# Kernel tuning notes

Measured on AMD Instinct MI355X. Metric: run time of the kernel, lower is better.

The kernel has to match this reference:

```python
import jax, jax.numpy as jnp
import numpy as np
from jax import lax

ALPHA = 0.85
C1 = 0.01 ** 2
C2 = 0.03 ** 2


def _avg_pool3(x):
    # F.avg_pool2d(x, 3, 1, 1) with count_include_pad=True: zero-pad, divide by 9.
    s = lax.reduce_window(x, jnp.array(0.0, x.dtype), lax.add,
                          (1, 1, 3, 3), (1, 1, 1, 1),
                          [(0, 0), (0, 0), (1, 1), (1, 1)])
    return s / jnp.array(9.0, x.dtype)


def _ssim(x, y):
    mu_x = _avg_pool3(x)
    mu_y = _avg_pool3(y)
    sigma_x = jnp.clip(_avg_pool3(x * x) - mu_x * mu_x, 0.0, None)
    sigma_y = jnp.clip(_avg_pool3(y * y) - mu_y * mu_y, 0.0, None)
    sigma_xy = _avg_pool3(x * y) - mu_x * mu_y
    ssim_n = (2.0 * mu_x * mu_y + C1) * (2.0 * sigma_xy + C2)
    ssim_d = (mu_x * mu_x + mu_y * mu_y + C1) * (sigma_x + sigma_y + C2)
    return jnp.clip((1.0 - ssim_n / ssim_d) / 2.0, 0.0, 1.0)


def _warp_right(right_img, disp):
    # grid_sample(bilinear, border, align_corners=True) where y maps identically
    # to its own row -> a 1D horizontal bilinear gather at x_sample = x - disp.
    B, C, H, W = right_img.shape
    x_base = jnp.arange(W, dtype=disp.dtype).reshape(1, 1, 1, W)
    x_sample = x_base - disp                      # [B,1,H,W]
    xs = jnp.clip(x_sample, 0.0, W - 1.0)         # border padding
    x0 = jnp.floor(xs)
    w = xs - x0                                   # frac weight
    i0 = x0.astype(jnp.int32)
    i1 = jnp.minimum(i0 + 1, W - 1)
    i0b = jnp.broadcast_to(i0, (B, C, H, W))
    i1b = jnp.broadcast_to(i1, (B, C, H, W))
    g0 = jnp.take_along_axis(right_img, i0b, axis=3)
    g1 = jnp.take_along_axis(right_img, i1b, axis=3)
    warped = (1.0 - w) * g0 + w * g1              # w broadcasts over C
    valid = ((x_sample > 0) & (x_sample < W - 1)).astype(disp.dtype)
    return warped, valid


def setup_inputs() -> dict:
    key = jax.random.key(0)
    k1, k2, k3 = jax.random.split(key, 3)
    B, H, W = 8, 720, 1280
    disp = jax.random.normal(k1, (B, 1, H, W), dtype=jnp.float32)
    left_img = jax.random.uniform(k2, (B, 3, H, W), dtype=jnp.float32)
    right_img = jax.random.uniform(k3, (B, 3, H, W), dtype=jnp.float32)
    return {"disp": disp, "left_img": left_img, "right_img": right_img}


def reference(disp, left_img, right_img):
    right_warped, valid = _warp_right(right_img, disp)
    l1_err = jnp.mean(jnp.abs(left_img - right_warped), axis=1, keepdims=True)
    ssim_err = jnp.mean(_ssim(left_img, right_warped), axis=1, keepdims=True)
    photo_err = ALPHA * ssim_err + (1.0 - ALPHA) * l1_err
    n_valid = jnp.maximum(jnp.sum(valid), 1.0)
    return jnp.sum(photo_err * valid) / n_valid
```

## Files before the change

### kernel.cpp

```cpp
#include <hip/hip_runtime.h>


#define P_ALPHA 0.85f
#define P_C1 1e-4f
#define P_C2 9e-4f

constexpr int COLS  = 62;
constexpr int RPW   = 15;
constexpr int WAVES = 4;

__global__ __launch_bounds__(256, 4)
void photo_loss_kernel(const float* __restrict__ disp,
                       const float* __restrict__ left,
                       const float* __restrict__ right,
                       float* __restrict__ acc,
                       int H, int W)
{
    __shared__ float redpv[WAVES];
    __shared__ float redv[WAVES];

    const int tid  = threadIdx.x;
    const int lane = tid & 63;
    const int w    = tid >> 6;
    const int b    = blockIdx.z;
    const int col  = blockIdx.x * COLS + lane - 1;
    const int rowStart = (blockIdx.y * WAVES + w) * RPW;

    const int planeHW = H * W;
    const float* __restrict__ dispb = disp  + b * planeHW;
    const float* __restrict__ L0 = left  + (b * 3 + 0) * planeHW;
    const float* __restrict__ L1 = left  + (b * 3 + 1) * planeHW;
    const float* __restrict__ L2 = left  + (b * 3 + 2) * planeHW;
    const float* __restrict__ R0 = right + (b * 3 + 0) * planeHW;
    const float* __restrict__ R1 = right + (b * 3 + 1) * planeHW;
    const float* __restrict__ R2 = right + (b * 3 + 2) * planeHW;

    const float wm1f = (float)(W - 1);
    const int   colC = min(max(col, 0), W - 1);
    const float colv = (col >= 0 && col < W) ? 1.f : 0.f;
    const float ocm  = (lane >= 1 && lane <= COLS && col < W) ? 1.f : 0.f;

    float rsx[3][3], rsy[3][3], rsxx[3][3], rsyy[3][3], rsxy[3][3];
    float l1r[3], vr[3];

    float sum_pv = 0.f, sum_v = 0.f;

    auto emit = [&](int cs) {
        const float inv9 = 1.f / 9.f;
        float ssim_sum = 0.f;
        #pragma unroll
        for (int c = 0; c < 3; ++c) {
            float mu_x = (rsx[c][0]  + rsx[c][1]  + rsx[c][2])  * inv9;
            float mu_y = (rsy[c][0]  + rsy[c][1]  + rsy[c][2])  * inv9;
            float exx  = (rsxx[c][0] + rsxx[c][1] + rsxx[c][2]) * inv9;
            float eyy  = (rsyy[c][0] + rsyy[c][1] + rsyy[c][2]) * inv9;
            float exy  = (rsxy[c][0] + rsxy[c][1] + rsxy[c][2]) * inv9;
            float sig_x  = fmaxf(exx - mu_x * mu_x, 0.f);
            float sig_y  = fmaxf(eyy - mu_y * mu_y, 0.f);
            float sig_xy = exy - mu_x * mu_y;
            float n  = (2.f * mu_x * mu_y + P_C1) * (2.f * sig_xy + P_C2);
            float dd = (mu_x * mu_x + mu_y * mu_y + P_C1) * (sig_x + sig_y + P_C2);
            float s  = (1.f - n * __builtin_amdgcn_rcpf(dd)) * 0.5f;
            s = fminf(fmaxf(s, 0.f), 1.f);
            ssim_sum += s;
        }
        float photo = P_ALPHA * (ssim_sum * (1.f / 3.f))
                    + (1.f - P_ALPHA) * (l1r[cs] * (1.f / 3.f));
        sum_pv += photo * vr[cs] * ocm;
        sum_v  += vr[cs] * ocm;
    };

    float gC0,gC1,gC2,gC3,gC4,gC5, frC, vmC;
    float xC0,xC1,xC2;
    float dN;
    int   offN;

    {
        const int r0   = rowStart - 1;
        const int rc0  = max(r0, 0);
        const int off0 = rc0 * W + colC;
        const float d0 = dispb[off0];
        xC0 = L0[off0]; xC1 = L1[off0]; xC2 = L2[off0];
        offN = rowStart * W + colC;
        dN = dispb[offN];
        const float xs  = (float)col - d0;
        const float xcl = fminf(fmaxf(xs, 0.f), wm1f);
        const float xf  = floorf(xcl);
        frC = xcl - xf;
        const int i0 = (int)xf;
        const int i1 = min(i0 + 1, W - 1);
        const int ro = rc0 * W;
        gC0 = R0[ro + i0]; gC1 = R0[ro + i1];
        gC2 = R1[ro + i0]; gC3 = R1[ro + i1];
        gC4 = R2[ro + i0]; gC5 = R2[ro + i1];
        vmC = (xs > 0.f && xs < wm1f) ? 1.f : 0.f;
    }

    #pragma unroll
    for (int j = 0; j <= RPW + 2; ++j) {
        const int s = j % 3;
        const int r = rowStart - 1 + j;
        if (j <= RPW + 1) {
            float gN0=0.f,gN1=0.f,gN2=0.f,gN3=0.f,gN4=0.f,gN5=0.f, frN=0.f, vmN=0.f;
            float xN0=0.f,xN1=0.f,xN2=0.f, dF=0.f;
            int   offF = 0;
            if (j <= RPW) {
                const float xs  = (float)col - dN;
                const float xcl = fminf(fmaxf(xs, 0.f), wm1f);
                const float xf  = floorf(xcl);
                frN = xcl - xf;
                const int i0 = (int)xf;
                const int i1 = min(i0 + 1, W - 1);
                const int ro = offN - colC;
                gN0 = R0[ro + i0]; gN1 = R0[ro + i1];
                gN2 = R1[ro + i0]; gN3 = R1[ro + i1];
                gN4 = R2[ro + i0]; gN5 = R2[ro + i1];
                vmN = (xs > 0.f && xs < wm1f) ? 1.f : 0.f;

                xN0 = L0[offN]; xN1 = L1[offN]; xN2 = L2[offN];
                const int rc2 = min(r + 2, H - 1);
                offF = rc2 * W + colC;
                dF = dispb[offF];
            }

            if (j >= 3) emit((s + 1) % 3);

            const float rv = (r >= 0 && r < H) ? 1.f : 0.f;
            const float m  = rv * colv;
            const float omf = 1.f - frC;
            const float y0 = (omf * gC0 + frC * gC1) * m;
            const float y1 = (omf * gC2 + frC * gC3) * m;
            const float y2 = (omf * gC4 + frC * gC5) * m;
            const float x0 = xC0 * m;
            const float x1 = xC1 * m;
            const float x2 = xC2 * m;

            float xl, xr, yl, yr;
            xl = __shfl_up(x0, 1, 64); xr = __shfl_down(x0, 1, 64);
            yl = __shfl_up(y0, 1, 64); yr = __shfl_down(y0, 1, 64);
            rsx[0][s]  = xl + x0 + xr;
            rsy[0][s]  = yl + y0 + yr;
            rsxx[0][s] = xl * xl + x0 * x0 + xr * xr;
            rsyy[0][s] = yl * yl + y0 * y0 + yr * yr;
            rsxy[0][s] = xl * yl + x0 * y0 + xr * yr;

            xl = __shfl_up(x1, 1, 64); xr = __shfl_down(x1, 1, 64);
            yl = __shfl_up(y1, 1, 64); yr = __shfl_down(y1, 1, 64);
            rsx[1][s]  = xl + x1 + xr;
            rsy[1][s]  = yl + y1 + yr;
            rsxx[1][s] = xl * xl + x1 * x1 + xr * xr;
            rsyy[1][s] = yl * yl + y1 * y1 + yr * yr;
            rsxy[1][s] = xl * yl + x1 * y1 + xr * yr;

            xl = __shfl_up(x2, 1, 64); xr = __shfl_down(x2, 1, 64);
            yl = __shfl_up(y2, 1, 64); yr = __shfl_down(y2, 1, 64);
            rsx[2][s]  = xl + x2 + xr;
            rsy[2][s]  = yl + y2 + yr;
            rsxx[2][s] = xl * xl + x2 * x2 + xr * xr;
            rsyy[2][s] = yl * yl + y2 * y2 + yr * yr;
            rsxy[2][s] = xl * yl + x2 * y2 + xr * yr;

            l1r[s] = fabsf(x0 - y0) + fabsf(x1 - y1) + fabsf(x2 - y2);
            vr[s]  = vmC;

            if (j <= RPW) {
                gC0 = gN0; gC1 = gN1; gC2 = gN2; gC3 = gN3; gC4 = gN4; gC5 = gN5;
                frC = frN; vmC = vmN;
                xC0 = xN0; xC1 = xN1; xC2 = xN2;
                dN = dF; offN = offF;
            }
        } else {
            emit((s + 1) % 3);
        }
    }

    #pragma unroll
    for (int off = 32; off > 0; off >>= 1) {
        sum_pv += __shfl_down(sum_pv, off, 64);
        sum_v  += __shfl_down(sum_v,  off, 64);
    }
    if (lane == 0) { redpv[w] = sum_pv; redv[w] = sum_v; }
    __syncthreads();
    if (tid == 0) {
        atomicAdd(&acc[0], redpv[0] + redpv[1] + redpv[2] + redpv[3]);
        atomicAdd(&acc[1], redv[0]  + redv[1]  + redv[2]  + redv[3]);
    }
}

__global__ void photo_loss_finalize(const float* __restrict__ acc,
                                    float* __restrict__ out)
{
    out[0] = acc[0] / fmaxf(acc[1], 1.f);
}

extern "C" void kernel_launch(void* const* d_in, const int* in_sizes, int n_in,
                              void* d_out, int out_size, void* d_ws, size_t ws_size,
                              hipStream_t stream)
{
    const float* disp  = (const float*)d_in[0];
    const float* left  = (const float*)d_in[1];
    const float* right = (const float*)d_in[2];
    float* out = (float*)d_out;
    float* acc = (float*)d_ws;

    const int B = 8, H = 720, W = 1280;

    hipMemsetAsync(acc, 0, 2 * sizeof(float), stream);

    dim3 grid((W + COLS - 1) / COLS, H / (WAVES * RPW), B);
    dim3 block(256);
    photo_loss_kernel<<<grid, block, 0, stream>>>(disp, left, right, acc, H, W);
    photo_loss_finalize<<<1, 1, 0, stream>>>(acc, out);
}
```

Measured before the change: 239.7 us.

## Restructure row loop as rolling named-register window with partial unroll and higher occupancy

Replaces the fully unrolled 3-slot ring buffer of row sums with explicit A/B/C named register sets that shift each iteration, uses unroll 2 instead of full unroll, and emits SSIM for the middle row as soon as the current row is computed. The launch bound is raised to 6 blocks per SIMD-group target to force lower register use and more waves in flight for latency hiding of the gather loads. Risks include extra register moves per iteration, possible spilling under the tighter bound, and loop overhead from partial unrolling.

```diff
diff --git a/kernel.cpp b/kernel.cpp
--- a/kernel.cpp
+++ b/kernel.cpp
@@ -9,7 +9,7 @@
 constexpr int RPW   = 15;
 constexpr int WAVES = 4;
 
-__global__ __launch_bounds__(256, 4)
+__global__ __launch_bounds__(256, 6)
 void photo_loss_kernel(const float* __restrict__ disp,
                        const float* __restrict__ left,
                        const float* __restrict__ right,
@@ -40,138 +40,145 @@
     const float colv = (col >= 0 && col < W) ? 1.f : 0.f;
     const float ocm  = (lane >= 1 && lane <= COLS && col < W) ? 1.f : 0.f;
 
-    float rsx[3][3], rsy[3][3], rsxx[3][3], rsyy[3][3], rsxy[3][3];
-    float l1r[3], vr[3];
+    float Ax0=0.f,Ay0=0.f,Axx0=0.f,Ayy0=0.f,Axy0=0.f;
+    float Ax1=0.f,Ay1=0.f,Axx1=0.f,Ayy1=0.f,Axy1=0.f;
+    float Ax2=0.f,Ay2=0.f,Axx2=0.f,Ayy2=0.f,Axy2=0.f;
+    float Bx0=0.f,By0=0.f,Bxx0=0.f,Byy0=0.f,Bxy0=0.f;
+    float Bx1=0.f,By1=0.f,Bxx1=0.f,Byy1=0.f,Bxy1=0.f;
+    float Bx2=0.f,By2=0.f,Bxx2=0.f,Byy2=0.f,Bxy2=0.f;
+    float l1P=0.f, vP=0.f;
 
     float sum_pv = 0.f, sum_v = 0.f;
 
-    auto emit = [&](int cs) {
-        const float inv9 = 1.f / 9.f;
-        float ssim_sum = 0.f;
-        #pragma unroll
-        for (int c = 0; c < 3; ++c) {
-            float mu_x = (rsx[c][0]  + rsx[c][1]  + rsx[c][2])  * inv9;
-            float mu_y = (rsy[c][0]  + rsy[c][1]  + rsy[c][2])  * inv9;
-            float exx  = (rsxx[c][0] + rsxx[c][1] + rsxx[c][2]) * inv9;
-            float eyy  = (rsyy[c][0] + rsyy[c][1] + rsyy[c][2]) * inv9;
-            float exy  = (rsxy[c][0] + rsxy[c][1] + rsxy[c][2]) * inv9;
-            float sig_x  = fmaxf(exx - mu_x * mu_x, 0.f);
-            float sig_y  = fmaxf(eyy - mu_y * mu_y, 0.f);
-            float sig_xy = exy - mu_x * mu_y;
-            float n  = (2.f * mu_x * mu_y + P_C1) * (2.f * sig_xy + P_C2);
-            float dd = (mu_x * mu_x + mu_y * mu_y + P_C1) * (sig_x + sig_y + P_C2);
-            float s  = (1.f - n * __builtin_amdgcn_rcpf(dd)) * 0.5f;
-            s = fminf(fmaxf(s, 0.f), 1.f);
-            ssim_sum += s;
-        }
-        float photo = P_ALPHA * (ssim_sum * (1.f / 3.f))
-                    + (1.f - P_ALPHA) * (l1r[cs] * (1.f / 3.f));
-        sum_pv += photo * vr[cs] * ocm;
-        sum_v  += vr[cs] * ocm;
-    };
-
-    float gC0,gC1,gC2,gC3,gC4,gC5, frC, vmC;
-    float xC0,xC1,xC2;
+    float gN0,gN1,gN2,gN3,gN4,gN5, frN, vmN, xN0,xN1,xN2;
     float dN;
     int   offN;
 
     {
-        const int r0   = rowStart - 1;
-        const int rc0  = max(r0, 0);
-        const int off0 = rc0 * W + colC;
-        const float d0 = dispb[off0];
-        xC0 = L0[off0]; xC1 = L1[off0]; xC2 = L2[off0];
+        const int   rc0  = max(rowStart - 1, 0);
+        const int   off0 = rc0 * W + colC;
+        const float d0   = dispb[off0];
+        xN0 = L0[off0]; xN1 = L1[off0]; xN2 = L2[off0];
         offN = rowStart * W + colC;
-        dN = dispb[offN];
+        dN   = dispb[offN];
         const float xs  = (float)col - d0;
         const float xcl = fminf(fmaxf(xs, 0.f), wm1f);
         const float xf  = floorf(xcl);
-        frC = xcl - xf;
+        frN = xcl - xf;
         const int i0 = (int)xf;
         const int i1 = min(i0 + 1, W - 1);
         const int ro = rc0 * W;
-        gC0 = R0[ro + i0]; gC1 = R0[ro + i1];
-        gC2 = R1[ro + i0]; gC3 = R1[ro + i1];
-        gC4 = R2[ro + i0]; gC5 = R2[ro + i1];
-        vmC = (xs > 0.f && xs < wm1f) ? 1.f : 0.f;
-    }
-
-    #pragma unroll
-    for (int j = 0; j <= RPW + 2; ++j) {
-        const int s = j % 3;
+        gN0 = R0[ro + i0]; gN1 = R0[ro + i1];
+        gN2 = R1[ro + i0]; gN3 = R1[ro + i1];
+        gN4 = R2[ro + i0]; gN5 = R2[ro + i1];
+        vmN = (xs > 0.f && xs < wm1f) ? 1.f : 0.f;
+    }
+
+    #pragma unroll 2
+    for (int j = 0; j < RPW + 2; ++j) {
         const int r = rowStart - 1 + j;
-        if (j <= RPW + 1) {
-            float gN0=0.f,gN1=0.f,gN2=0.f,gN3=0.f,gN4=0.f,gN5=0.f, frN=0.f, vmN=0.f;
-            float xN0=0.f,xN1=0.f,xN2=0.f, dF=0.f;
-            int   offF = 0;
-            if (j <= RPW) {
-                const float xs  = (float)col - dN;
-                const float xcl = fminf(fmaxf(xs, 0.f), wm1f);
-                const float xf  = floorf(xcl);
-                frN = xcl - xf;
-                const int i0 = (int)xf;
-                const int i1 = min(i0 + 1, W - 1);
-                const int ro = offN - colC;
-                gN0 = R0[ro + i0]; gN1 = R0[ro + i1];
-                gN2 = R1[ro + i0]; gN3 = R1[ro + i1];
-                gN4 = R2[ro + i0]; gN5 = R2[ro + i1];
-                vmN = (xs > 0.f && xs < wm1f) ? 1.f : 0.f;
-
-                xN0 = L0[offN]; xN1 = L1[offN]; xN2 = L2[offN];
-                const int rc2 = min(r + 2, H - 1);
-                offF = rc2 * W + colC;
-                dF = dispb[offF];
+
+        const float g0=gN0,g1=gN1,g2=gN2,g3=gN3,g4=gN4,g5=gN5;
+        const float fr=frN, vm=vmN, xc0=xN0, xc1=xN1, xc2=xN2;
+
+        if (j <= RPW) {
+            const float xs  = (float)col - dN;
+            const float xcl = fminf(fmaxf(xs, 0.f), wm1f);
+            const float xf  = floorf(xcl);
+            frN = xcl - xf;
+            const int i0 = (int)xf;
+            const int i1 = min(i0 + 1, W - 1);
+            const int ro = offN - colC;
+            gN0 = R0[ro + i0]; gN1 = R0[ro + i1];
+            gN2 = R1[ro + i0]; gN3 = R1[ro + i1];
+            gN4 = R2[ro + i0]; gN5 = R2[ro + i1];
+            vmN = (xs > 0.f && xs < wm1f) ? 1.f : 0.f;
+            xN0 = L0[offN]; xN1 = L1[offN]; xN2 = L2[offN];
+            const int rc2 = min(r + 2, H - 1);
+            offN = rc2 * W + colC;
+            dN   = dispb[offN];
+        }
+
+        const float rv  = (r >= 0 && r < H) ? 1.f : 0.f;
+        const float m   = rv * colv;
+        const float omf = 1.f - fr;
+        const float y0 = (omf * g0 + fr * g1) * m;
+        const float y1 = (omf * g2 + fr * g3) * m;
+        const float y2 = (omf * g4 + fr * g5) * m;
+        const float x0 = xc0 * m;
+        const float x1 = xc1 * m;
+        const float x2 = xc2 * m;
+
+        float Cx0,Cy0,Cxx0,Cyy0,Cxy0;
+        float Cx1,Cy1,Cxx1,Cyy1,Cxy1;
+        float Cx2,Cy2,Cxx2,Cyy2,Cxy2;
+        {
+            const float xl = __shfl_up(x0,1,64), xr = __shfl_down(x0,1,64);
+            const float yl = __shfl_up(y0,1,64), yr = __shfl_down(y0,1,64);
+            Cx0  = xl + x0 + xr;
+            Cy0  = yl + y0 + yr;
+            Cxx0 = xl*xl + x0*x0 + xr*xr;
+            Cyy0 = yl*yl + y0*y0 + yr*yr;
+            Cxy0 = xl*yl + x0*y0 + xr*yr;
+        }
+        {
+            const float xl = __shfl_up(x1,1,64), xr = __shfl_down(x1,1,64);
+            const float yl = __shfl_up(y1,1,64), yr = __shfl_down(y1,1,64);
+            Cx1  = xl + x1 + xr;
+            Cy1  = yl + y1 + yr;
+            Cxx1 = xl*xl + x1*x1 + xr*xr;
+            Cyy1 = yl*yl + y1*y1 + yr*yr;
+            Cxy1 = xl*yl + x1*y1 + xr*yr;
+        }
+        {
+            const float xl = __shfl_up(x2,1,64), xr = __shfl_down(x2,1,64);
+            const float yl = __shfl_up(y2,1,64), yr = __shfl_down(y2,1,64);
+            Cx2  = xl + x2 + xr;
+            Cy2  = yl + y2 + yr;
+            Cxx2 = xl*xl + x2*x2 + xr*xr;
+            Cyy2 = yl*yl + y2*y2 + yr*yr;
+            Cxy2 = xl*yl + x2*y2 + xr*yr;
+        }
+        const float l1C = fabsf(x0 - y0) + fabsf(x1 - y1) + fabsf(x2 - y2);
+        const float vC  = vm;
+
+        if (j >= 2) {
+            const float inv9 = 1.f / 9.f;
+            float ssim_sum = 0.f;
+            #define SSIM_CH(SX,SY,SXX,SYY,SXY)                                   \
+            {                                                                    \
+                const float mu_x = (A##SX + B##SX + C##SX) * inv9;               \
+                const float mu_y = (A##SY + B##SY + C##SY) * inv9;               \
+                const float exx  = (A##SXX + B##SXX + C##SXX) * inv9;            \
+                const float eyy  = (A##SYY + B##SYY + C##SYY) * inv9;            \
+                const float exy  = (A##SXY + B##SXY + C##SXY) * inv9;            \
+                const float sig_x  = fmaxf(exx - mu_x * mu_x, 0.f);              \
+                const float sig_y  = fmaxf(eyy - mu_y * mu_y, 0.f);              \
+                const float sig_xy = exy - mu_x * mu_y;                          \
+                const float n  = (2.f*mu_x*mu_y + P_C1) * (2.f*sig_xy + P_C2);   \
+                const float dd = (mu_x*mu_x + mu_y*mu_y + P_C1)                  \
+                               * (sig_x + sig_y + P_C2);                         \
+                float s = (1.f - n * __builtin_amdgcn_rcpf(dd)) * 0.5f;          \
+                s = fminf(fmaxf(s, 0.f), 1.f);                                   \
+                ssim_sum += s;                                                   \
             }
-
-            if (j >= 3) emit((s + 1) % 3);
-
-            const float rv = (r >= 0 && r < H) ? 1.f : 0.f;
-            const float m  = rv * colv;
-            const float omf = 1.f - frC;
-            const float y0 = (omf * gC0 + frC * gC1) * m;
-            const float y1 = (omf * gC2 + frC * gC3) * m;
-            const float y2 = (omf * gC4 + frC * gC5) * m;
-            const float x0 = xC0 * m;
-            const float x1 = xC1 * m;
-            const float x2 = xC2 * m;
-
-            float xl, xr, yl, yr;
-            xl = __shfl_up(x0, 1, 64); xr = __shfl_down(x0, 1, 64);
-            yl = __shfl_up(y0, 1, 64); yr = __shfl_down(y0, 1, 64);
-            rsx[0][s]  = xl + x0 + xr;
-            rsy[0][s]  = yl + y0 + yr;
-            rsxx[0][s] = xl * xl + x0 * x0 + xr * xr;
-            rsyy[0][s] = yl * yl + y0 * y0 + yr * yr;
-            rsxy[0][s] = xl * yl + x0 * y0 + xr * yr;
-
-            xl = __shfl_up(x1, 1, 64); xr = __shfl_down(x1, 1, 64);
-            yl = __shfl_up(y1, 1, 64); yr = __shfl_down(y1, 1, 64);
-            rsx[1][s]  = xl + x1 + xr;
-            rsy[1][s]  = yl + y1 + yr;
-            rsxx[1][s] = xl * xl + x1 * x1 + xr * xr;
-            rsyy[1][s] = yl * yl + y1 * y1 + yr * yr;
-            rsxy[1][s] = xl * yl + x1 * y1 + xr * yr;
-
-            xl = __shfl_up(x2, 1, 64); xr = __shfl_down(x2, 1, 64);
-            yl = __shfl_up(y2, 1, 64); yr = __shfl_down(y2, 1, 64);
-            rsx[2][s]  = xl + x2 + xr;
-            rsy[2][s]  = yl + y2 + yr;
-            rsxx[2][s] = xl * xl + x2 * x2 + xr * xr;
-            rsyy[2][s] = yl * yl + y2 * y2 + yr * yr;
-            rsxy[2][s] = xl * yl + x2 * y2 + xr * yr;
-
-            l1r[s] = fabsf(x0 - y0) + fabsf(x1 - y1) + fabsf(x2 - y2);
-            vr[s]  = vmC;
-
-            if (j <= RPW) {
-                gC0 = gN0; gC1 = gN1; gC2 = gN2; gC3 = gN3; gC4 = gN4; gC5 = gN5;
-                frC = frN; vmC = vmN;
-                xC0 = xN0; xC1 = xN1; xC2 = xN2;
-                dN = dF; offN = offF;
-            }
-        } else {
-            emit((s + 1) % 3);
-        }
+            SSIM_CH(x0,y0,xx0,yy0,xy0)
+            SSIM_CH(x1,y1,xx1,yy1,xy1)
+            SSIM_CH(x2,y2,xx2,yy2,xy2)
+            #undef SSIM_CH
+            const float photo = P_ALPHA * (ssim_sum * (1.f / 3.f))
+                              + (1.f - P_ALPHA) * (l1P * (1.f / 3.f));
+            sum_pv += photo * vP * ocm;
+            sum_v  += vP * ocm;
+        }
+
+        Ax0=Bx0; Ay0=By0; Axx0=Bxx0; Ayy0=Byy0; Axy0=Bxy0;
+        Ax1=Bx1; Ay1=By1; Axx1=Bxx1; Ayy1=Byy1; Axy1=Bxy1;
+        Ax2=Bx2; Ay2=By2; Axx2=Bxx2; Ayy2=Byy2; Axy2=Bxy2;
+        Bx0=Cx0; By0=Cy0; Bxx0=Cxx0; Byy0=Cyy0; Bxy0=Cxy0;
+        Bx1=Cx1; By1=Cy1; Bxx1=Cxx1; Byy1=Cyy1; Bxy1=Cxy1;
+        Bx2=Cx2; By2=Cy2; Bxx2=Cxx2; Byy2=Cyy2; Bxy2=Cxy2;
+        l1P = l1C; vP = vC;
     }
 
     #pragma unroll
```

After: 260.8 us. 1.09x slower.
